# Kernel tuning notes

Measured on AMD Instinct MI355X. Metric: run time of the kernel, lower is better.

## Reference

```python
import jax, jax.numpy as jnp
import numpy as np

DIM = 1024
N_HEADS = 16
HEAD_DIM = DIM // N_HEADS  # 64
B, T = 4, 2048


def setup_inputs() -> dict:
    key = jax.random.key(0)
    ks = jax.random.split(key, 6)
    x = jax.random.normal(ks[0], (B, T, DIM), dtype=jnp.float32)
    # causal mask; original does att.masked_fill(mask == 0, -inf)
    mask = jnp.tril(jnp.ones((T, T), dtype=bool))[None, None, :, :]
    s = 1.0 / np.sqrt(DIM)
    Wq = jax.random.normal(ks[1], (DIM, DIM), dtype=jnp.float32) * s
    Wk = jax.random.normal(ks[2], (DIM, DIM), dtype=jnp.float32) * s
    Wv = jax.random.normal(ks[3], (DIM, DIM), dtype=jnp.float32) * s
    Wo = jax.random.normal(ks[4], (DIM, DIM), dtype=jnp.float32) * s
    bo = jnp.zeros((DIM,), dtype=jnp.float32)
    return {"x": x, "mask": mask, "Wq": Wq, "Wk": Wk, "Wv": Wv,
            "Wo": Wo, "bo": bo, "start_pos": 0}


def reference(x, mask, Wq, Wk, Wv, Wo, bo, start_pos):
    Bx, Tx, C = x.shape
    # torch nn.Linear: y = x @ W.T (no bias for QKV)
    q = jnp.einsum('btc,dc->btd', x, Wq).reshape(Bx, Tx, N_HEADS, HEAD_DIM)
    k = jnp.einsum('btc,dc->btd', x, Wk).reshape(Bx, Tx, N_HEADS, HEAD_DIM)
    v = jnp.einsum('btc,dc->btd', x, Wv).reshape(Bx, Tx, N_HEADS, HEAD_DIM)
    # no caching path: keys=k, values=v
    scale = 1.0 / jnp.sqrt(jnp.asarray(HEAD_DIM, dtype=x.dtype))
    # [B, H, Tq, Tk]
    att = jnp.einsum('bqhd,bkhd->bhqk', q, k) * scale
    att = jnp.where(mask, att, jnp.asarray(-jnp.inf, dtype=att.dtype))
    att = jax.nn.softmax(att, axis=-1)
    out = jnp.einsum('bhqk,bkhd->bqhd', att, v).reshape(Bx, Tx, C)
    return jnp.einsum('btc,dc->btd', out, Wo) + bo
```

## Files before the change

kernel.cpp:

```cpp
#include <hip/hip_runtime.h>
#include <cstdint>
#include <cstddef>

typedef __bf16 bf16;
typedef bf16 bf16x8 __attribute__((ext_vector_type(8)));
typedef float f32x4 __attribute__((ext_vector_type(4)));

__device__ inline f32x4 mfma_16x16x32(bf16x8 a, bf16x8 b, f32x4 c) {
    return __builtin_amdgcn_mfma_f32_16x16x32_bf16(a, b, c, 0, 0, 0);
}

#define GLD16(gsrc, ldst)                                                              \
    __builtin_amdgcn_global_load_lds(                                                  \
        (const __attribute__((address_space(1))) uint32_t*)(gsrc),                     \
        (__attribute__((address_space(3))) uint32_t*)(ldst), 16, 0, 0)

__global__ void cvt_kernel(const float* __restrict__ src, bf16* __restrict__ dst, int n) {
    int i = (blockIdx.x * blockDim.x + threadIdx.x) * 4;
    if (i >= n) return;
    float4 f = *(const float4*)(src + i);
    union { bf16 o4[4]; uint2 u; } pk;
    pk.o4[0] = (bf16)f.x; pk.o4[1] = (bf16)f.y; pk.o4[2] = (bf16)f.z; pk.o4[3] = (bf16)f.w;
    *(uint2*)(dst + i) = pk.u;
}

__global__ void cvt4_kernel(const float* __restrict__ s0, const float* __restrict__ s1,
                            const float* __restrict__ s2, const float* __restrict__ s3,
                            bf16* __restrict__ d0, bf16* __restrict__ d1,
                            bf16* __restrict__ d2, bf16* __restrict__ d3) {
    const int z = blockIdx.y;
    const float* src = (z == 0) ? s0 : (z == 1) ? s1 : (z == 2) ? s2 : s3;
    bf16* dst = (z == 0) ? d0 : (z == 1) ? d1 : (z == 2) ? d2 : d3;
    int i = (blockIdx.x * blockDim.x + threadIdx.x) * 4;
    float4 f = *(const float4*)(src + i);
    union { bf16 o4[4]; uint2 u; } pk;
    pk.o4[0] = (bf16)f.x; pk.o4[1] = (bf16)f.y; pk.o4[2] = (bf16)f.z; pk.o4[3] = (bf16)f.w;
    *(uint2*)(dst + i) = pk.u;
}

#define BM 128
#define BN 128
#define BK 64
#define QSCALE 0.18033688011112042f

__global__ __launch_bounds__(256, 2)
void gemm_qkv(const bf16* __restrict__ xb,
              const bf16* __restrict__ wq, const bf16* __restrict__ wk, const bf16* __restrict__ wv,
              bf16* __restrict__ qo, bf16* __restrict__ ko, bf16* __restrict__ vo)
{
    __shared__ bf16 sA[BM][BK];
    __shared__ bf16 sB[BN][BK];
    const int K = 1024;
    const int tid = threadIdx.x;
    const int lane = tid & 63, wave = tid >> 6;
    const int wm = wave >> 1, wn = wave & 1;
    const int quad = lane >> 4, ln = lane & 15;
    const int lr = lane >> 3;
    const int ssc = ((lane & 7) ^ lr) * 8;
    const int lnm = ln & 7;
    const int rc0 = (quad ^ lnm) * 8;
    const int rc1 = ((4 | quad) ^ lnm) * 8;
    const int id = blockIdx.x;
    const int z = id >> 9;
    const int xt = (id & 511) >> 6;
    const int yt = id & 63;
    const bf16* W = (z == 0) ? wq : (z == 1) ? wk : wv;
    const int row0 = yt * BM;
    const int col0 = xt * BN;

    f32x4 acc[4][4];
    const f32x4 zero = {0.f, 0.f, 0.f, 0.f};
#pragma unroll
    for (int i = 0; i < 4; ++i)
#pragma unroll
        for (int j = 0; j < 4; ++j) acc[i][j] = zero;

    for (int k0 = 0; k0 < K; k0 += BK) {
#pragma unroll
        for (int s = 0; s < 4; ++s) {
            int ra = wave * 32 + s * 8;
            GLD16(&xb[(size_t)(row0 + ra + lr) * K + k0 + ssc], &sA[ra][0]);
            GLD16(&W [(size_t)(col0 + ra + lr) * K + k0 + ssc], &sB[ra][0]);
        }
        __syncthreads();
#pragma unroll
        for (int kk = 0; kk < BK; kk += 32) {
            const int rc = kk ? rc1 : rc0;
            bf16x8 af[4], bfv[4];
#pragma unroll
            for (int i = 0; i < 4; ++i) {
                af[i]  = *(const bf16x8*)(&sA[wm * 64 + i * 16 + ln][rc]);
                bfv[i] = *(const bf16x8*)(&sB[wn * 64 + i * 16 + ln][rc]);
            }
#pragma unroll
            for (int mi = 0; mi < 4; ++mi)
#pragma unroll
                for (int ni = 0; ni < 4; ++ni)
                    acc[mi][ni] = mfma_16x16x32(af[mi], bfv[ni], acc[mi][ni]);
        }
        __syncthreads();
    }
    if (z == 2) {
#pragma unroll
        for (int mi = 0; mi < 4; ++mi)
#pragma unroll
            for (int ni = 0; ni < 4; ++ni) {
                int gm0 = row0 + wm * 64 + mi * 16 + quad * 4;
                int gn = col0 + wn * 64 + ni * 16 + ln;
                int b = gm0 >> 11, t = gm0 & 2047;
                int h = gn >> 6,  d = gn & 63;
                union { bf16 v[4]; uint2 u; } pk;
#pragma unroll
                for (int i = 0; i < 4; ++i) pk.v[i] = (bf16)acc[mi][ni][i];
                *(uint2*)(&vo[((size_t)((b * 16 + h) * 64 + d)) * 2048 + t]) = pk.u;
            }
    } else {
        const float scale = (z == 0) ? QSCALE : 1.0f;
        bf16* outp = (z == 0) ? qo : ko;
#pragma unroll
        for (int mi = 0; mi < 4; ++mi)
#pragma unroll
            for (int ni = 0; ni < 4; ++ni)
#pragma unroll
                for (int i = 0; i < 4; ++i) {
                    int gm = row0 + wm * 64 + mi * 16 + quad * 4 + i;
                    int gn = col0 + wn * 64 + ni * 16 + ln;
                    int b = gm >> 11, t = gm & 2047;
                    int h = gn >> 6,  d = gn & 63;
                    outp[((size_t)((b * 16 + h) * 2048 + t)) * 64 + d] = (bf16)(acc[mi][ni][i] * scale);
                }
    }
}

__global__ __launch_bounds__(256, 2)
void gemm_out(const bf16* __restrict__ ab, const bf16* __restrict__ wo,
              const float* __restrict__ bias, float* __restrict__ out)
{
    __shared__ bf16 sA[BM][BK];
    __shared__ bf16 sB[BN][BK];
    const int K = 1024;
    const int tid = threadIdx.x;
    const int lane = tid & 63, wave = tid >> 6;
    const int wm = wave >> 1, wn = wave & 1;
    const int quad = lane >> 4, ln = lane & 15;
    const int lr = lane >> 3;
    const int ssc = ((lane & 7) ^ lr) * 8;
    const int lnm = ln & 7;
    const int rc0 = (quad ^ lnm) * 8;
    const int rc1 = ((4 | quad) ^ lnm) * 8;
    const int id = blockIdx.x;
    const int xt = id >> 6, yt = id & 63;
    const int row0 = yt * BM;
    const int col0 = xt * BN;

    f32x4 acc[4][4];
    const f32x4 zero = {0.f, 0.f, 0.f, 0.f};
#pragma unroll
    for (int i = 0; i < 4; ++i)
#pragma unroll
        for (int j = 0; j < 4; ++j) acc[i][j] = zero;

    for (int k0 = 0; k0 < K; k0 += BK) {
#pragma unroll
        for (int s = 0; s < 4; ++s) {
            int ra = wave * 32 + s * 8;
            GLD16(&ab[(size_t)(row0 + ra + lr) * K + k0 + ssc], &sA[ra][0]);
            GLD16(&wo[(size_t)(col0 + ra + lr) * K + k0 + ssc], &sB[ra][0]);
        }
        __syncthreads();
#pragma unroll
        for (int kk = 0; kk < BK; kk += 32) {
            const int rc = kk ? rc1 : rc0;
            bf16x8 af[4], bfv[4];
#pragma unroll
            for (int i = 0; i < 4; ++i) {
                af[i]  = *(const bf16x8*)(&sA[wm * 64 + i * 16 + ln][rc]);
                bfv[i] = *(const bf16x8*)(&sB[wn * 64 + i * 16 + ln][rc]);
            }
#pragma unroll
            for (int mi = 0; mi < 4; ++mi)
#pragma unroll
                for (int ni = 0; ni < 4; ++ni)
                    acc[mi][ni] = mfma_16x16x32(af[mi], bfv[ni], acc[mi][ni]);
        }
        __syncthreads();
    }
#pragma unroll
    for (int mi = 0; mi < 4; ++mi)
#pragma unroll
        for (int ni = 0; ni < 4; ++ni)
#pragma unroll
            for (int i = 0; i < 4; ++i) {
                int gm = row0 + wm * 64 + mi * 16 + quad * 4 + i;
                int gn = col0 + wn * 64 + ni * 16 + ln;
                out[(size_t)gm * 1024 + gn] = acc[mi][ni][i] + bias[gn];
            }
}

__global__ __launch_bounds__(256, 2)
void flash_attn(const bf16* __restrict__ q, const bf16* __restrict__ k,
                const bf16* __restrict__ vt, bf16* __restrict__ ao)
{
    __shared__ bf16 sK[64][72];
    __shared__ bf16 sV[64][72];
    __shared__ bf16 sP[4][32][72];
    const int tid = threadIdx.x, lane = tid & 63, w = tid >> 6;
    const int quad = lane >> 4, ln = lane & 15;
    const int id = blockIdx.x;
    const int bh = id & 63;
    const int q0 = (15 - (id >> 6)) * 128;
    const size_t base = (size_t)bh * (2048 * 64);
    const int sr = tid >> 3, sc = (tid & 7) * 8;
    const int rw = q0 + w * 32;

    bf16x8 qf[2][2];
#pragma unroll
    for (int mi = 0; mi < 2; ++mi)
#pragma unroll
        for (int kf = 0; kf < 2; ++kf)
            qf[mi][kf] = *(const bf16x8*)(&q[base + (size_t)(rw + mi * 16 + ln) * 64 + kf * 32 + quad * 8]);

    const f32x4 zero = {0.f, 0.f, 0.f, 0.f};
    f32x4 o[2][4];
    float lsum[2][4];
#pragma unroll
    for (int mi = 0; mi < 2; ++mi)
#pragma unroll
        for (int j = 0; j < 4; ++j) { o[mi][j] = zero; lsum[mi][j] = 0.f; }

    const int kend = q0 + 128;
    uint4 rKa = *(const uint4*)(&k [base + (size_t)sr * 64 + sc]);
    uint4 rKb = *(const uint4*)(&k [base + (size_t)(sr + 32) * 64 + sc]);
    uint4 rVa = *(const uint4*)(&vt[base + (size_t)sr * 2048 + sc]);
    uint4 rVb = *(const uint4*)(&vt[base + (size_t)(sr + 32) * 2048 + sc]);

    for (int k0 = 0; k0 < kend; k0 += 64) {
        __syncthreads();
        *(uint4*)(&sK[sr][sc])      = rKa;
        *(uint4*)(&sK[sr + 32][sc]) = rKb;
        *(uint4*)(&sV[sr][sc])      = rVa;
        *(uint4*)(&sV[sr + 32][sc]) = rVb;
        __syncthreads();
        if (k0 + 64 < kend) {
            int kn = k0 + 64;
            rKa = *(const uint4*)(&k [base + (size_t)(kn + sr) * 64 + sc]);
            rKb = *(const uint4*)(&k [base + (size_t)(kn + sr + 32) * 64 + sc]);
            rVa = *(const uint4*)(&vt[base + (size_t)sr * 2048 + kn + sc]);
            rVb = *(const uint4*)(&vt[base + (size_t)(sr + 32) * 2048 + kn + sc]);
        }
        if (k0 <= rw + 31) {
            const bool diag = (k0 + 63 > rw);
            bf16x8 kb[4][2];
#pragma unroll
            for (int nt = 0; nt < 4; ++nt)
#pragma unroll
                for (int kf = 0; kf < 2; ++kf)
                    kb[nt][kf] = *(const bf16x8*)(&sK[nt * 16 + ln][kf * 32 + quad * 8]);
            f32x4 s[2][4];
#pragma unroll
            for (int mi = 0; mi < 2; ++mi)
#pragma unroll
                for (int nt = 0; nt < 4; ++nt) {
                    f32x4 a = zero;
                    a = mfma_16x16x32(qf[mi][0], kb[nt][0], a);
                    a = mfma_16x16x32(qf[mi][1], kb[nt][1], a);
                    s[mi][nt] = a;
                }
#pragma unroll
            for (int mi = 0; mi < 2; ++mi)
#pragma unroll
                for (int i = 0; i < 4; ++i) {
                    const int row = rw + mi * 16 + quad * 4 + i;
                    float ps = 0.f;
#pragma unroll
                    for (int nt = 0; nt < 4; ++nt) {
                        float sv = s[mi][nt][i];
                        if (diag) {
                            int col = k0 + nt * 16 + ln;
                            sv = (col > row) ? -INFINITY : sv;
                        }
                        float p = __builtin_amdgcn_exp2f(sv);
                        ps += p;
                        sP[w][mi * 16 + quad * 4 + i][nt * 16 + ln] = (bf16)p;
                    }
                    lsum[mi][i] += ps;
                }
            bf16x8 ap[2][2], vb[4][2];
#pragma unroll
            for (int mi = 0; mi < 2; ++mi)
#pragma unroll
                for (int kf = 0; kf < 2; ++kf)
                    ap[mi][kf] = *(const bf16x8*)(&sP[w][mi * 16 + ln][kf * 32 + quad * 8]);
#pragma unroll
            for (int nt = 0; nt < 4; ++nt)
#pragma unroll
                for (int kf = 0; kf < 2; ++kf)
                    vb[nt][kf] = *(const bf16x8*)(&sV[nt * 16 + ln][kf * 32 + quad * 8]);
#pragma unroll
            for (int mi = 0; mi < 2; ++mi)
#pragma unroll
                for (int nt = 0; nt < 4; ++nt) {
                    o[mi][nt] = mfma_16x16x32(ap[mi][0], vb[nt][0], o[mi][nt]);
                    o[mi][nt] = mfma_16x16x32(ap[mi][1], vb[nt][1], o[mi][nt]);
                }
        }
    }

    const int b = bh >> 4, h = bh & 15;
#pragma unroll
    for (int mi = 0; mi < 2; ++mi) {
        const int rb = rw + mi * 16;
        float inv[4];
#pragma unroll
        for (int i = 0; i < 4; ++i) {
            float l = lsum[mi][i];
#pragma unroll
            for (int off = 1; off < 16; off <<= 1) l += __shfl_xor(l, off);
            inv[i] = 1.0f / l;
        }
#pragma unroll
        for (int i = 0; i < 4; ++i)
#pragma unroll
            for (int nt = 0; nt < 4; ++nt)
                sP[w][mi * 16 + quad * 4 + i][nt * 16 + ln] = (bf16)(o[mi][nt][i] * inv[i]);
#pragma unroll
        for (int p = 0; p < 2; ++p) {
            const int row = p * 8 + (lane >> 3);
            uint4 val = *(const uint4*)(&sP[w][mi * 16 + row][(lane & 7) * 8]);
            *(uint4*)(&ao[(size_t)(b * 2048 + rb + row) * 1024 + h * 64 + (lane & 7) * 8]) = val;
        }
    }
}

extern "C" void kernel_launch(void* const* d_in, const int* in_sizes, int n_in,
                              void* d_out, int out_size, void* d_ws, size_t ws_size,
                              hipStream_t stream) {
    const float* x  = (const float*)d_in[0];
    const float* Wq = (const float*)d_in[2];
    const float* Wk = (const float*)d_in[3];
    const float* Wv = (const float*)d_in[4];
    const float* Wo = (const float*)d_in[5];
    const float* bo = (const float*)d_in[6];
    float* out = (float*)d_out;

    char* p = (char*)d_ws;
    const size_t MK = 8192ull * 1024;
    bf16* xb  = (bf16*)p; p += MK * 2;
    bf16* wqb = (bf16*)p; p += (1ull << 20) * 2;
    bf16* wkb = (bf16*)p; p += (1ull << 20) * 2;
    bf16* wvb = (bf16*)p; p += (1ull << 20) * 2;
    bf16* wob = (bf16*)p; p += (1ull << 20) * 2;
    bf16* qb  = (bf16*)p; p += MK * 2;
    bf16* kb  = (bf16*)p; p += MK * 2;
    bf16* vtb = (bf16*)p; p += MK * 2;
    bf16* aob = (bf16*)p; p += MK * 2;

    cvt_kernel<<<(int)(MK / 1024), 256, 0, stream>>>(x, xb, (int)MK);
    cvt4_kernel<<<dim3(1024, 4), 256, 0, stream>>>(Wq, Wk, Wv, Wo, wqb, wkb, wvb, wob);

    gemm_qkv<<<1536, 256, 0, stream>>>(xb, wqb, wkb, wvb, qb, kb, vtb);
    flash_attn<<<1024, 256, 0, stream>>>(qb, kb, vtb, aob);
    gemm_out<<<512, 256, 0, stream>>>(aob, wob, bo, out);
}
```

Measured before the change: 245.0 us.

## Use 32x32 MFMA with transposed scores to keep P in registers

Rewrites the flash-attention inner loop to use 32x32x16 bf16 MFMA, computing S^T = K·Q^T so each lane holds a single query row's scores. The probabilities are packed to bf16 and rearranged between lane halves with permlane32_swap, so they feed the PV MFMA directly instead of passing through the sP shared buffer. Key tiles that lie entirely above the causal diagonal are skipped at 32-column granularity. This removes LDS traffic for P and the 16-lane row-sum reductions, at the cost of a larger accumulator register footprint and a less coalesced output store.

New measurement: 230.5 us. 1.06x faster.

```diff
diff --git a/kernel.cpp b/kernel.cpp
--- a/kernel.cpp
+++ b/kernel.cpp
@@ -5,9 +5,18 @@
 typedef __bf16 bf16;
 typedef bf16 bf16x8 __attribute__((ext_vector_type(8)));
 typedef float f32x4 __attribute__((ext_vector_type(4)));
+typedef float f32x16 __attribute__((ext_vector_type(16)));
 
 __device__ inline f32x4 mfma_16x16x32(bf16x8 a, bf16x8 b, f32x4 c) {
     return __builtin_amdgcn_mfma_f32_16x16x32_bf16(a, b, c, 0, 0, 0);
+}
+__device__ inline f32x16 mfma_32x32x16(bf16x8 a, bf16x8 b, f32x16 c) {
+    return __builtin_amdgcn_mfma_f32_32x32x16_bf16(a, b, c, 0, 0, 0);
+}
+__device__ inline uint32_t cvt_pk_bf16(float lo, float hi) {
+    uint32_t r;
+    asm("v_cvt_pk_bf16_f32 %0, %1, %2" : "=v"(r) : "v"(lo), "v"(hi));
+    return r;
 }
 
 #define GLD16(gsrc, ldst)                                                              \
@@ -203,30 +212,25 @@
 {
     __shared__ bf16 sK[64][72];
     __shared__ bf16 sV[64][72];
-    __shared__ bf16 sP[4][32][72];
     const int tid = threadIdx.x, lane = tid & 63, w = tid >> 6;
-    const int quad = lane >> 4, ln = lane & 15;
+    const int c31 = lane & 31, hi = lane >> 5, hi8 = hi * 8;
     const int id = blockIdx.x;
     const int bh = id & 63;
     const int q0 = (15 - (id >> 6)) * 128;
     const size_t base = (size_t)bh * (2048 * 64);
     const int sr = tid >> 3, sc = (tid & 7) * 8;
     const int rw = q0 + w * 32;
-
-    bf16x8 qf[2][2];
-#pragma unroll
-    for (int mi = 0; mi < 2; ++mi)
-#pragma unroll
-        for (int kf = 0; kf < 2; ++kf)
-            qf[mi][kf] = *(const bf16x8*)(&q[base + (size_t)(rw + mi * 16 + ln) * 64 + kf * 32 + quad * 8]);
-
-    const f32x4 zero = {0.f, 0.f, 0.f, 0.f};
-    f32x4 o[2][4];
-    float lsum[2][4];
-#pragma unroll
-    for (int mi = 0; mi < 2; ++mi)
-#pragma unroll
-        for (int j = 0; j < 4; ++j) { o[mi][j] = zero; lsum[mi][j] = 0.f; }
+    const int rw31 = rw + 31;
+    const int qrow = rw + c31;
+
+    bf16x8 qf[4];
+#pragma unroll
+    for (int dt = 0; dt < 4; ++dt)
+        qf[dt] = *(const bf16x8*)(&q[base + (size_t)qrow * 64 + dt * 16 + hi8]);
+
+    const f32x16 z16 = {0.f,0.f,0.f,0.f,0.f,0.f,0.f,0.f,0.f,0.f,0.f,0.f,0.f,0.f,0.f,0.f};
+    f32x16 o0 = z16, o1 = z16;
+    float lsum = 0.f;
 
     const int kend = q0 + 128;
     uint4 rKa = *(const uint4*)(&k [base + (size_t)sr * 64 + sc]);
@@ -248,87 +252,74 @@
             rVa = *(const uint4*)(&vt[base + (size_t)sr * 2048 + kn + sc]);
             rVb = *(const uint4*)(&vt[base + (size_t)(sr + 32) * 2048 + kn + sc]);
         }
-        if (k0 <= rw + 31) {
-            const bool diag = (k0 + 63 > rw);
-            bf16x8 kb[4][2];
-#pragma unroll
-            for (int nt = 0; nt < 4; ++nt)
-#pragma unroll
-                for (int kf = 0; kf < 2; ++kf)
-                    kb[nt][kf] = *(const bf16x8*)(&sK[nt * 16 + ln][kf * 32 + quad * 8]);
-            f32x4 s[2][4];
-#pragma unroll
-            for (int mi = 0; mi < 2; ++mi)
-#pragma unroll
-                for (int nt = 0; nt < 4; ++nt) {
-                    f32x4 a = zero;
-                    a = mfma_16x16x32(qf[mi][0], kb[nt][0], a);
-                    a = mfma_16x16x32(qf[mi][1], kb[nt][1], a);
-                    s[mi][nt] = a;
+        if (k0 <= rw31) {
+#pragma unroll
+            for (int kt = 0; kt < 2; ++kt) {
+                const int ktb = k0 + kt * 32;
+                if (ktb <= rw31) {
+                    bf16x8 kf0 = *(const bf16x8*)(&sK[kt * 32 + c31][ 0 + hi8]);
+                    bf16x8 kf1 = *(const bf16x8*)(&sK[kt * 32 + c31][16 + hi8]);
+                    bf16x8 kf2 = *(const bf16x8*)(&sK[kt * 32 + c31][32 + hi8]);
+                    bf16x8 kf3 = *(const bf16x8*)(&sK[kt * 32 + c31][48 + hi8]);
+                    f32x16 st = z16;
+                    st = mfma_32x32x16(kf0, qf[0], st);
+                    st = mfma_32x32x16(kf1, qf[1], st);
+                    st = mfma_32x32x16(kf2, qf[2], st);
+                    st = mfma_32x32x16(kf3, qf[3], st);
+                    const int kb2 = ktb + hi * 4;
+                    if (ktb + 31 > rw) {
+#pragma unroll
+                        for (int r = 0; r < 16; ++r) {
+                            int kk = kb2 + (r & 3) + 8 * (r >> 2);
+                            if (kk > qrow) st[r] = -INFINITY;
+                        }
+                    }
+                    float pp[16];
+                    float ps = 0.f;
+#pragma unroll
+                    for (int r = 0; r < 16; ++r) {
+                        float p = __builtin_amdgcn_exp2f(st[r]);
+                        ps += p;
+                        pp[r] = p;
+                    }
+                    lsum += ps;
+#pragma unroll
+                    for (int ks = 0; ks < 2; ++ks) {
+                        const int ob = ks * 8;
+                        uint32_t a0 = cvt_pk_bf16(pp[ob + 0], pp[ob + 1]);
+                        uint32_t a1 = cvt_pk_bf16(pp[ob + 2], pp[ob + 3]);
+                        uint32_t a2 = cvt_pk_bf16(pp[ob + 4], pp[ob + 5]);
+                        uint32_t a3 = cvt_pk_bf16(pp[ob + 6], pp[ob + 7]);
+                        auto r02 = __builtin_amdgcn_permlane32_swap(a0, a2, false, false);
+                        auto r13 = __builtin_amdgcn_permlane32_swap(a1, a3, false, false);
+                        union { uint32_t u[4]; bf16x8 v; } af;
+                        af.u[0] = r02[0]; af.u[1] = r13[0];
+                        af.u[2] = r02[1]; af.u[3] = r13[1];
+                        const int co = kt * 32 + ks * 16 + hi8;
+                        bf16x8 v0 = *(const bf16x8*)(&sV[c31][co]);
+                        bf16x8 v1 = *(const bf16x8*)(&sV[32 + c31][co]);
+                        o0 = mfma_32x32x16(v0, af.v, o0);
+                        o1 = mfma_32x32x16(v1, af.v, o1);
+                    }
                 }
-#pragma unroll
-            for (int mi = 0; mi < 2; ++mi)
-#pragma unroll
-                for (int i = 0; i < 4; ++i) {
-                    const int row = rw + mi * 16 + quad * 4 + i;
-                    float ps = 0.f;
-#pragma unroll
-                    for (int nt = 0; nt < 4; ++nt) {
-                        float sv = s[mi][nt][i];
-                        if (diag) {
-                            int col = k0 + nt * 16 + ln;
-                            sv = (col > row) ? -INFINITY : sv;
-                        }
-                        float p = __builtin_amdgcn_exp2f(sv);
-                        ps += p;
-                        sP[w][mi * 16 + quad * 4 + i][nt * 16 + ln] = (bf16)p;
-                    }
-                    lsum[mi][i] += ps;
-                }
-            bf16x8 ap[2][2], vb[4][2];
-#pragma unroll
-            for (int mi = 0; mi < 2; ++mi)
-#pragma unroll
-                for (int kf = 0; kf < 2; ++kf)
-                    ap[mi][kf] = *(const bf16x8*)(&sP[w][mi * 16 + ln][kf * 32 + quad * 8]);
-#pragma unroll
-            for (int nt = 0; nt < 4; ++nt)
-#pragma unroll
-                for (int kf = 0; kf < 2; ++kf)
-                    vb[nt][kf] = *(const bf16x8*)(&sV[nt * 16 + ln][kf * 32 + quad * 8]);
-#pragma unroll
-            for (int mi = 0; mi < 2; ++mi)
-#pragma unroll
-                for (int nt = 0; nt < 4; ++nt) {
-                    o[mi][nt] = mfma_16x16x32(ap[mi][0], vb[nt][0], o[mi][nt]);
-                    o[mi][nt] = mfma_16x16x32(ap[mi][1], vb[nt][1], o[mi][nt]);
-                }
-        }
-    }
-
+            }
+        }
+    }
+
+    float l = lsum + __shfl_xor(lsum, 32);
+    const float inv = 1.0f / l;
     const int b = bh >> 4, h = bh & 15;
-#pragma unroll
-    for (int mi = 0; mi < 2; ++mi) {
-        const int rb = rw + mi * 16;
-        float inv[4];
+    bf16* orow = &ao[(size_t)(b * 2048 + qrow) * 1024 + h * 64];
+#pragma unroll
+    for (int g = 0; g < 4; ++g) {
+        union { bf16 v4[4]; uint2 u; } pk0, pk1;
 #pragma unroll
         for (int i = 0; i < 4; ++i) {
-            float l = lsum[mi][i];
-#pragma unroll
-            for (int off = 1; off < 16; off <<= 1) l += __shfl_xor(l, off);
-            inv[i] = 1.0f / l;
-        }
-#pragma unroll
-        for (int i = 0; i < 4; ++i)
-#pragma unroll
-            for (int nt = 0; nt < 4; ++nt)
-                sP[w][mi * 16 + quad * 4 + i][nt * 16 + ln] = (bf16)(o[mi][nt][i] * inv[i]);
-#pragma unroll
-        for (int p = 0; p < 2; ++p) {
-            const int row = p * 8 + (lane >> 3);
-            uint4 val = *(const uint4*)(&sP[w][mi * 16 + row][(lane & 7) * 8]);
-            *(uint4*)(&ao[(size_t)(b * 2048 + rb + row) * 1024 + h * 64 + (lane & 7) * 8]) = val;
-        }
+            pk0.v4[i] = (bf16)(o0[g * 4 + i] * inv);
+            pk1.v4[i] = (bf16)(o1[g * 4 + i] * inv);
+        }
+        *(uint2*)(&orow[     g * 8 + hi * 4]) = pk0.u;
+        *(uint2*)(&orow[32 + g * 8 + hi * 4]) = pk1.u;
     }
 }
 
```
